# Optimization experiments

Measured on AMD Instinct MI355X. Metric: run time of the kernel, lower is better.

The kernel has to match this reference:

```python
import jax, jax.numpy as jnp
import numpy as np

RES = 32            # input grid resolution
OUT_RES = 64        # after subdivide
C = 128             # channels (== out_channels -> skip is identity)
G = 32              # group-norm groups
N = 8192            # active input voxels
EPS = 1e-5

# 8 child offsets for subdivide, 27 stencil offsets for 3x3x3 submanifold conv
_OFFS8 = np.stack(np.meshgrid([0, 1], [0, 1], [0, 1], indexing='ij'), -1).reshape(-1, 3).astype(np.int32)
_OFFS27 = np.stack(np.meshgrid([-1, 0, 1], [-1, 0, 1], [-1, 0, 1], indexing='ij'), -1).reshape(-1, 3).astype(np.int32)


def group_norm(x, gamma, beta, num_groups=G, eps=EPS):
    # sparse group norm over all active voxels of the (single) sample
    n, c = x.shape
    xg = x.reshape(n, num_groups, c // num_groups)
    mean = xg.mean(axis=(0, 2), keepdims=True)
    var = xg.var(axis=(0, 2), keepdims=True)
    xn = (xg - mean) * jax.lax.rsqrt(var + eps)
    return xn.reshape(n, c) * gamma + beta


def subdivide_coords(coords):
    offs = jnp.asarray(_OFFS8)
    return (coords[:, None, :] * 2 + offs[None, :, :]).reshape(-1, 3)  # [8N, 3]


def subm_conv3d(feats, coords, W, b, grid_res):
    # submanifold 3x3x3 sparse conv: outputs only at active sites
    n = feats.shape[0]
    grid = jnp.full((grid_res, grid_res, grid_res), -1, dtype=jnp.int32)
    grid = grid.at[coords[:, 0], coords[:, 1], coords[:, 2]].set(
        jnp.arange(n, dtype=jnp.int32))
    out = jnp.zeros((n, W.shape[-1]), dtype=feats.dtype)
    for k in range(27):  # fixed small stencil loop
        off = jnp.asarray(_OFFS27[k])
        nb = coords + off
        inb = jnp.all((nb >= 0) & (nb < grid_res), axis=1)
        nbc = jnp.clip(nb, 0, grid_res - 1)
        idx = grid[nbc[:, 0], nbc[:, 1], nbc[:, 2]]
        mask = inb & (idx >= 0)
        g = jnp.where(mask[:, None], feats[jnp.where(mask, idx, 0)], 0.0)
        out = out + g @ W[k]
    return out + b


def setup_inputs() -> dict:
    key = jax.random.key(0)
    ks = jax.random.split(key, 8)
    rng = np.random.default_rng(0)
    flat = rng.choice(RES ** 3, size=N, replace=False)
    coords = np.stack([flat // (RES * RES), (flat // RES) % RES, flat % RES],
                      axis=-1).astype(np.int32)
    feats = jax.random.normal(ks[0], (N, C), dtype=jnp.float32)
    gamma1 = 1.0 + 0.1 * jax.random.normal(ks[1], (C,), dtype=jnp.float32)
    beta1 = 0.1 * jax.random.normal(ks[2], (C,), dtype=jnp.float32)
    W1 = jax.random.normal(ks[3], (27, C, C), dtype=jnp.float32) * 0.05
    b1 = jax.random.normal(ks[4], (C,), dtype=jnp.float32) * 0.05
    gamma2 = 1.0 + 0.1 * jax.random.normal(ks[5], (C,), dtype=jnp.float32)
    beta2 = 0.1 * jax.random.normal(ks[6], (C,), dtype=jnp.float32)
    W2 = jax.random.normal(ks[7], (27, C, C), dtype=jnp.float32) * 0.05
    b2 = jax.random.normal(jax.random.fold_in(key, 99), (C,), dtype=jnp.float32) * 0.05
    return {"feats": feats, "gamma1": gamma1, "beta1": beta1, "W1": W1,
            "b1": b1, "gamma2": gamma2, "beta2": beta2, "W2": W2, "b2": b2,
            "coords": jnp.asarray(coords)}


def reference(feats, gamma1, beta1, W1, b1, gamma2, beta2, W2, b2, coords):
    # act_layers: GroupNorm + SiLU at input resolution
    h = jax.nn.silu(group_norm(feats, gamma1, beta1))
    # subdivide both branch and residual (8 children per voxel)
    new_coords = subdivide_coords(coords)          # [8N, 3] in OUT_RES grid
    h = jnp.repeat(h, 8, axis=0)
    x_sub = jnp.repeat(feats, 8, axis=0)
    # out_layers: conv3 -> GN -> SiLU -> conv3 (submanifold, same active set)
    h = subm_conv3d(h, new_coords, W1, b1, OUT_RES)
    h = jax.nn.silu(group_norm(h, gamma2, beta2))
    h = subm_conv3d(h, new_coords, W2, b2, OUT_RES)
    # skip_connection is Identity since out_channels == channels
    return h + x_sub
```

## Files before the change

kernel.cpp:

```cpp
#include <hip/hip_runtime.h>

#define NPAR   8192
#define NCH    65536
#define RES    32
#define EPS    1e-5f

typedef __attribute__((ext_vector_type(8))) short short8;
typedef __attribute__((ext_vector_type(4))) float floatx4;

__device__ __forceinline__ unsigned short f2bf(float f) {
    union { float f; unsigned u; } v; v.f = f;
    unsigned r = v.u + 0x7fffu + ((v.u >> 16) & 1u);
    return (unsigned short)(r >> 16);
}
__device__ __forceinline__ float bf2f(unsigned short b) {
    union { unsigned u; float f; } v; v.u = ((unsigned)b) << 16;
    return v.f;
}
__device__ __forceinline__ void glds16(const void* g, void* l) {
    __builtin_amdgcn_global_load_lds(
        (__attribute__((address_space(1))) const void*)g,
        (__attribute__((address_space(3))) void*)l, 16, 0, 0);
}
__device__ __forceinline__ int k27_of(int o, int s) {
    return (((o >> 2) & 1) + ((s >> 2) & 1)) * 9 +
           (((o >> 1) & 1) + ((s >> 1) & 1)) * 3 +
           ((o & 1) + (s & 1));
}
__device__ __forceinline__ void axis_dlist(int o, int s, int* d, int& n) {
    if (o == 0) { if (s == 0) { d[0] = -1; n = 1; } else { d[0] = 0; d[1] = 1; n = 2; } }
    else        { if (s == 0) { d[0] = -1; d[1] = 0; n = 2; } else { d[0] = 1; n = 1; } }
}

__global__ void k1_kernel(const int* __restrict__ coords, int* __restrict__ grid32,
                          const float* __restrict__ x, float* __restrict__ sum,
                          float* __restrict__ sq) {
    int b = blockIdx.x;
    int t = threadIdx.x;
    if (b < 32) {
        int p = b * 256 + t;
        grid32[(coords[p*3] << 10) + (coords[p*3+1] << 5) + coords[p*3+2]] = p;
    } else {
        __shared__ float s_sum[32], s_sq[32];
        if (t < 32) { s_sum[t] = 0.0f; s_sq[t] = 0.0f; }
        __syncthreads();
        const float4* x4 = (const float4*)x;
        int total = NPAR * 32;
        int idx0 = (b - 32) * 256 + t;
        int g = idx0 & 31;
        float ls = 0.0f, lq = 0.0f;
        for (int idx = idx0; idx < total; idx += 256 * 256) {
            float4 v = x4[idx];
            ls += v.x + v.y + v.z + v.w;
            lq += v.x * v.x + v.y * v.y + v.z * v.z + v.w * v.w;
        }
        atomicAdd(&s_sum[g], ls);
        atomicAdd(&s_sq[g], lq);
        __syncthreads();
        if (t < 32) { atomicAdd(&sum[t], s_sum[t]); atomicAdd(&sq[t], s_sq[t]); }
    }
}

__global__ void k2_kernel(const int* __restrict__ coords, const int* __restrict__ grid32,
                          int* __restrict__ idx_tab, int* __restrict__ pidx27,
                          const float* __restrict__ W1, const float* __restrict__ W2,
                          unsigned short* __restrict__ Wc1f, unsigned short* __restrict__ Wp2,
                          const float* __restrict__ x, const float* __restrict__ sum,
                          const float* __restrict__ sq, const float* __restrict__ gamma,
                          const float* __restrict__ beta, unsigned short* __restrict__ y) {
    int b = blockIdx.x;
    if (b < 256) {
        int R = b * 256 + threadIdx.x;
        int p = R >> 3, o = R & 7;
        int bx = 2 * coords[p*3]   + ((o >> 2) & 1);
        int by = 2 * coords[p*3+1] + ((o >> 1) & 1);
        int bz = 2 * coords[p*3+2] + (o & 1);
#pragma unroll 1
        for (int k = 0; k < 27; ++k) {
            int fx = bx + k / 9 - 1, fy = by + (k / 3) % 3 - 1, fz = bz + k % 3 - 1;
            int src = -1;
            if ((unsigned)fx < 64u && (unsigned)fy < 64u && (unsigned)fz < 64u) {
                int r = grid32[((fx >> 1) << 10) + ((fy >> 1) << 5) + (fz >> 1)];
                if ((unsigned)r < (unsigned)NPAR)
                    src = (((fx & 1) << 2) + ((fy & 1) << 1) + (fz & 1)) * NPAR + r;
            }
            idx_tab[k * NCH + R] = src;
        }
    } else if (b < 472) {
        int rem = (b - 256) * 256 + threadIdx.x;
        int lane = rem & 63;
        int ks   = (rem >> 6) & 3;
        int nb   = (rem >> 8) & 7;
        int tap  = rem >> 11;
        int n  = nb * 16 + (lane & 15);
        int k0 = ks * 32 + (lane >> 4) * 8;
        unsigned short v[8];
#pragma unroll
        for (int j = 0; j < 8; ++j) v[j] = f2bf(W2[tap * 16384 + (k0 + j) * 128 + n]);
        uint4 pk;
        pk.x = (unsigned)v[0] | ((unsigned)v[1] << 16);
        pk.y = (unsigned)v[2] | ((unsigned)v[3] << 16);
        pk.z = (unsigned)v[4] | ((unsigned)v[5] << 16);
        pk.w = (unsigned)v[6] | ((unsigned)v[7] << 16);
        *(uint4*)&Wp2[(long)rem * 8] = pk;
    } else if (b < 984) {
        int rem = (b - 472) * 256 + threadIdx.x;
        int lane  = rem & 63;
        int ks    = (rem >> 6) & 3;
        int nb    = (rem >> 8) & 7;
        int combo = rem >> 11;
        int o = combo >> 3, s = combo & 7;
        int n  = nb * 16 + (lane & 15);
        int k0 = ks * 32 + (lane >> 4) * 8;
        int d0[2], d1[2], d2[2], n0, n1, n2;
        axis_dlist((o >> 2) & 1, (s >> 2) & 1, d0, n0);
        axis_dlist((o >> 1) & 1, (s >> 1) & 1, d1, n1);
        axis_dlist(o & 1,        s & 1,        d2, n2);
        unsigned short v[8];
#pragma unroll
        for (int j = 0; j < 8; ++j) {
            float acc = 0.0f;
            for (int a = 0; a < n0; ++a)
                for (int bb = 0; bb < n1; ++bb)
                    for (int cc = 0; cc < n2; ++cc) {
                        int kk = (d0[a] + 1) * 9 + (d1[bb] + 1) * 3 + (d2[cc] + 1);
                        acc += W1[kk * 16384 + (k0 + j) * 128 + n];
                    }
            v[j] = f2bf(acc);
        }
        uint4 pk;
        pk.x = (unsigned)v[0] | ((unsigned)v[1] << 16);
        pk.y = (unsigned)v[2] | ((unsigned)v[3] << 16);
        pk.z = (unsigned)v[4] | ((unsigned)v[5] << 16);
        pk.w = (unsigned)v[6] | ((unsigned)v[7] << 16);
        *(uint4*)&Wc1f[(long)rem * 8] = pk;
    } else if (b < 1848) {
        int gid = (b - 984) * 256 + threadIdx.x;
        int k = gid >> 13, p = gid & 8191;
        int nx = coords[p*3]   + k / 9 - 1;
        int ny = coords[p*3+1] + (k / 3) % 3 - 1;
        int nz = coords[p*3+2] + k % 3 - 1;
        int src = -1;
        if ((unsigned)nx < 32u && (unsigned)ny < 32u && (unsigned)nz < 32u) {
            int r = grid32[(nx << 10) + (ny << 5) + nz];
            if ((unsigned)r < (unsigned)NPAR) src = r;
        }
        pidx27[k * NPAR + p] = src;
    } else {
        const float4* x4 = (const float4*)x;
        uint2* y2 = (uint2*)y;
        const float4* g4 = (const float4*)gamma;
        const float4* b4 = (const float4*)beta;
        float cnt = (float)NPAR * 4.0f;
        int total = NPAR * 32;
        for (int idx = (b - 1848) * 256 + threadIdx.x; idx < total; idx += 256 * 256) {
            int c4 = idx & 31;
            float mean = sum[c4] / cnt;
            float var = sq[c4] / cnt - mean * mean;
            float rstd = rsqrtf(var + EPS);
            float4 v = x4[idx];
            float4 gm = g4[c4];
            float4 bt = b4[c4];
            float a[4] = {v.x, v.y, v.z, v.w};
            float gg[4] = {gm.x, gm.y, gm.z, gm.w};
            float bb[4] = {bt.x, bt.y, bt.z, bt.w};
            unsigned short o[4];
#pragma unroll
            for (int i = 0; i < 4; ++i) {
                float tv = (a[i] - mean) * rstd * gg[i] + bb[i];
                o[i] = f2bf(tv / (1.0f + __expf(-tv)));
            }
            uint2 pk;
            pk.x = (unsigned)o[0] | ((unsigned)o[1] << 16);
            pk.y = (unsigned)o[2] | ((unsigned)o[3] << 16);
            y2[idx] = pk;
        }
    }
}

__global__ void gn_apply_bf16_kernel(unsigned short* __restrict__ x,
                                     const float* __restrict__ sum, const float* __restrict__ sq,
                                     const float* __restrict__ gamma, const float* __restrict__ beta,
                                     int nrows) {
    uint2* x2 = (uint2*)x;
    const float4* g4 = (const float4*)gamma;
    const float4* b4 = (const float4*)beta;
    float cnt = (float)nrows * 4.0f;
    int total = nrows * 32;
    for (int idx = blockIdx.x * blockDim.x + threadIdx.x; idx < total;
         idx += gridDim.x * blockDim.x) {
        int c4 = idx & 31;
        float mean = sum[c4] / cnt;
        float var = sq[c4] / cnt - mean * mean;
        float rstd = rsqrtf(var + EPS);
        uint2 pk = x2[idx];
        float a[4] = {bf2f((unsigned short)(pk.x & 0xffff)), bf2f((unsigned short)(pk.x >> 16)),
                      bf2f((unsigned short)(pk.y & 0xffff)), bf2f((unsigned short)(pk.y >> 16))};
        float4 gm = g4[c4];
        float4 bt = b4[c4];
        float gg[4] = {gm.x, gm.y, gm.z, gm.w};
        float bb[4] = {bt.x, bt.y, bt.z, bt.w};
        unsigned short o[4];
#pragma unroll
        for (int i = 0; i < 4; ++i) {
            float tv = (a[i] - mean) * rstd * gg[i] + bb[i];
            o[i] = f2bf(tv / (1.0f + __expf(-tv)));
        }
        pk.x = (unsigned)o[0] | ((unsigned)o[1] << 16);
        pk.y = (unsigned)o[2] | ((unsigned)o[3] << 16);
        x2[idx] = pk;
    }
}

__device__ __forceinline__ void mfma_phase(
    const unsigned short* __restrict__ Abuf, short8 (&bfr)[4][4],
    floatx4 (&acc)[4][4], int wm, int aswz) {
#pragma unroll
    for (int ks = 0; ks < 4; ++ks) {
        short8 afr[4];
#pragma unroll
        for (int mt = 0; mt < 4; ++mt)
            afr[mt] = *(const short8*)&Abuf[(wm << 13) + (mt << 11) + (ks << 9) + aswz];
#pragma unroll
        for (int mt = 0; mt < 4; ++mt)
#pragma unroll
            for (int nt = 0; nt < 4; ++nt)
                acc[mt][nt] = __builtin_amdgcn_mfma_f32_16x16x32_bf16(
                    afr[mt], bfr[nt][ks], acc[mt][nt], 0, 0, 0);
    }
}
__device__ __forceinline__ void loadB(const unsigned short* __restrict__ Wtap,
                                      short8 (&bfr)[4][4], int wn, int lane) {
#pragma unroll
    for (int nt = 0; nt < 4; ++nt)
#pragma unroll
        for (int ks = 0; ks < 4; ++ks)
            bfr[nt][ks] = *(const short8*)&Wtap[(((wn * 4 + nt) << 2) + ks) * 512 + (lane << 3)];
}
__device__ __forceinline__ void stageA(const unsigned short* __restrict__ Ag,
                                       int iv0, int iv1, const unsigned short* zsrc,
                                       unsigned short* __restrict__ buf,
                                       int base0, int base1, int cchOff) {
    const unsigned short* g0 = (iv0 >= 0) ? Ag + (long)iv0 * 128 : zsrc;
    const unsigned short* g1 = (iv1 >= 0) ? Ag + (long)iv1 * 128 : zsrc;
#pragma unroll
    for (int i = 0; i < 4; ++i) glds16(g0 + i * 32 + cchOff, &buf[base0 + i * 512]);
#pragma unroll
    for (int i = 0; i < 4; ++i) glds16(g1 + i * 32 + cchOff, &buf[base1 + i * 512]);
}

__global__ void __launch_bounds__(256, 2) conv1_fold_kernel(
    const unsigned short* __restrict__ Ag, const unsigned short* __restrict__ Wc1f,
    const float* __restrict__ bias, const int* __restrict__ pidx27,
    unsigned short* __restrict__ outp, const float* __restrict__ zpage,
    float* __restrict__ gsum, float* __restrict__ gsq) {
    __shared__ unsigned short A_lds[2][16384];

    int t = threadIdx.x;
    int o  = blockIdx.x & 7;
    int P0 = (blockIdx.x >> 3) << 7;
    const unsigned short* Wb = Wc1f + ((long)o << 17);
    int wv = t >> 6, lane = t & 63, quad = lane >> 4, l16 = lane & 15;
    int wm = wv & 1, wn = wv >> 1;
    int r16 = lane >> 2, cch = lane & 3;
    int c0 = wv * 2, c1 = wv * 2 + 1;
    int row0 = ((c0 >> 2) << 6) + ((c0 & 3) << 4) + r16;
    int row1 = ((c1 >> 2) << 6) + ((c1 & 3) << 4) + r16;
    int base0 = ((c0 >> 2) << 13) + ((c0 & 3) << 11);
    int base1 = ((c1 >> 2) << 13) + ((c1 & 3) << 11);
    int cchOff = (cch ^ ((r16 >> 1) & 3)) << 3;
    int aswz = (l16 << 5) + ((quad ^ ((l16 >> 1) & 3)) << 3);
    const unsigned short* zsrc = (const unsigned short*)zpage;

    floatx4 acc[4][4];
#pragma unroll
    for (int mt = 0; mt < 4; ++mt)
#pragma unroll
        for (int nt = 0; nt < 4; ++nt)
            acc[mt][nt] = (floatx4){0.f, 0.f, 0.f, 0.f};
    short8 bA[4][4], bB[4][4];

    stageA(Ag, pidx27[k27_of(o, 0) * NPAR + P0 + row0],
               pidx27[k27_of(o, 0) * NPAR + P0 + row1], zsrc, A_lds[0], base0, base1, cchOff);
    loadB(Wb, bA, wn, lane);
    int nv0 = pidx27[k27_of(o, 1) * NPAR + P0 + row0];
    int nv1 = pidx27[k27_of(o, 1) * NPAR + P0 + row1];
    __syncthreads();

#pragma unroll 1
    for (int s = 0; s < 8; s += 2) {
        stageA(Ag, nv0, nv1, zsrc, A_lds[1], base0, base1, cchOff);
        loadB(Wb + ((long)(s + 1) << 14), bB, wn, lane);
        if (s + 2 < 8) {
            nv0 = pidx27[k27_of(o, s + 2) * NPAR + P0 + row0];
            nv1 = pidx27[k27_of(o, s + 2) * NPAR + P0 + row1];
        }
        mfma_phase(A_lds[0], bA, acc, wm, aswz);
        __syncthreads();
        if (s + 2 < 8) {
            stageA(Ag, nv0, nv1, zsrc, A_lds[0], base0, base1, cchOff);
            loadB(Wb + ((long)(s + 2) << 14), bA, wn, lane);
            if (s + 3 < 8) {
                nv0 = pidx27[k27_of(o, s + 3) * NPAR + P0 + row0];
                nv1 = pidx27[k27_of(o, s + 3) * NPAR + P0 + row1];
            }
        }
        mfma_phase(A_lds[1], bB, acc, wm, aswz);
        __syncthreads();
    }

    float s_[4] = {0.f, 0.f, 0.f, 0.f}, q_[4] = {0.f, 0.f, 0.f, 0.f};
#pragma unroll
    for (int nt = 0; nt < 4; ++nt) {
        int col = wn * 64 + nt * 16 + l16;
        float bv = bias[col];
#pragma unroll
        for (int mt = 0; mt < 4; ++mt) {
#pragma unroll
            for (int r = 0; r < 4; ++r) {
                int prow = wm * 64 + mt * 16 + quad * 4 + r;
                long R = (long)o * NPAR + P0 + prow;
                float v = acc[mt][nt][r] + bv;
                unsigned short u = f2bf(v);
                outp[R * 128 + col] = u;
                float vr = bf2f(u);
                s_[nt] += vr;
                q_[nt] += vr * vr;
            }
        }
    }
    float* sred = (float*)A_lds;
    if (t < 64) sred[t] = 0.0f;
    __syncthreads();
#pragma unroll
    for (int nt = 0; nt < 4; ++nt) {
        int g = (wn * 64 + nt * 16 + l16) >> 2;
        atomicAdd(&sred[g], s_[nt]);
        atomicAdd(&sred[32 + g], q_[nt]);
    }
    __syncthreads();
    if (t < 32) { atomicAdd(&gsum[t], sred[t]); atomicAdd(&gsq[t], sred[32 + t]); }
}

__global__ void __launch_bounds__(256, 2) conv2_kernel(
    const unsigned short* __restrict__ Ag, const unsigned short* __restrict__ Wp,
    const float* __restrict__ bias, const int* __restrict__ idx_tab,
    const float* __restrict__ resid, float* __restrict__ outp,
    const float* __restrict__ zpage) {
    __shared__ unsigned short A_lds[2][16384];

    int t = threadIdx.x;
    int R0 = blockIdx.x * 128;
    int wv = t >> 6, lane = t & 63, quad = lane >> 4, l16 = lane & 15;
    int wm = wv & 1, wn = wv >> 1;
    int r16 = lane >> 2, cch = lane & 3;
    int c0 = wv * 2, c1 = wv * 2 + 1;
    int row0 = ((c0 >> 2) << 6) + ((c0 & 3) << 4) + r16;
    int row1 = ((c1 >> 2) << 6) + ((c1 & 3) << 4) + r16;
    int base0 = ((c0 >> 2) << 13) + ((c0 & 3) << 11);
    int base1 = ((c1 >> 2) << 13) + ((c1 & 3) << 11);
    int cchOff = (cch ^ ((r16 >> 1) & 3)) << 3;
    int aswz = (l16 << 5) + ((quad ^ ((l16 >> 1) & 3)) << 3);
    const unsigned short* zsrc = (const unsigned short*)zpage;

    floatx4 acc[4][4];
#pragma unroll
    for (int mt = 0; mt < 4; ++mt)
#pragma unroll
        for (int nt = 0; nt < 4; ++nt)
            acc[mt][nt] = (floatx4){0.f, 0.f, 0.f, 0.f};
    short8 bA[4][4], bB[4][4];

    stageA(Ag, idx_tab[R0 + row0], idx_tab[R0 + row1], zsrc, A_lds[0], base0, base1, cchOff);
    loadB(Wp, bA, wn, lane);
    int nv0 = idx_tab[NCH + R0 + row0], nv1 = idx_tab[NCH + R0 + row1];
    __syncthreads();

#pragma unroll 1
    for (int k = 0; k < 27; k += 2) {
        if (k + 1 < 27) {
            stageA(Ag, nv0, nv1, zsrc, A_lds[1], base0, base1, cchOff);
            loadB(Wp + ((long)(k + 1) << 14), bB, wn, lane);
            if (k + 2 < 27) {
                nv0 = idx_tab[(k + 2) * NCH + R0 + row0];
                nv1 = idx_tab[(k + 2) * NCH + R0 + row1];
            }
        }
        mfma_phase(A_lds[0], bA, acc, wm, aswz);
        __syncthreads();
        if (k + 1 < 27) {
            if (k + 2 < 27) {
                stageA(Ag, nv0, nv1, zsrc, A_lds[0], base0, base1, cchOff);
                loadB(Wp + ((long)(k + 2) << 14), bA, wn, lane);
                if (k + 3 < 27) {
                    nv0 = idx_tab[(k + 3) * NCH + R0 + row0];
                    nv1 = idx_tab[(k + 3) * NCH + R0 + row1];
                }
            }
            mfma_phase(A_lds[1], bB, acc, wm, aswz);
            __syncthreads();
        }
    }

#pragma unroll
    for (int nt = 0; nt < 4; ++nt) {
        int col = wn * 64 + nt * 16 + l16;
        float bv = bias[col];
#pragma unroll
        for (int mt = 0; mt < 4; ++mt) {
#pragma unroll
            for (int r = 0; r < 4; ++r) {
                int row = wm * 64 + mt * 16 + quad * 4 + r;
                long R = (long)R0 + row;
                float v = acc[mt][nt][r] + bv + resid[(R >> 3) * 128 + col];
                outp[R * 128 + col] = v;
            }
        }
    }
}

extern "C" void kernel_launch(void* const* d_in, const int* in_sizes, int n_in,
                              void* d_out, int out_size, void* d_ws, size_t ws_size,
                              hipStream_t stream) {
    const float* feats  = (const float*)d_in[0];
    const float* gamma1 = (const float*)d_in[1];
    const float* beta1  = (const float*)d_in[2];
    const float* W1     = (const float*)d_in[3];
    const float* b1     = (const float*)d_in[4];
    const float* gamma2 = (const float*)d_in[5];
    const float* beta2  = (const float*)d_in[6];
    const float* W2     = (const float*)d_in[7];
    const float* b2     = (const float*)d_in[8];
    const int*   coords = (const int*)d_in[9];
    float* out = (float*)d_out;

    char* ws = (char*)d_ws;
    unsigned short* h0b  = (unsigned short*)(ws);
    unsigned short* h1b  = (unsigned short*)(ws + (2u << 20));
    unsigned short* Wc1f = (unsigned short*)(ws + (18u << 20));
    unsigned short* Wp2  = (unsigned short*)(ws + (20u << 20));
    int*   grid32        = (int*)  (ws + (21u << 20));
    float* stats         = (float*)(ws + (21u << 20) + 131072);
    float* zpage         = (float*)(ws + (21u << 20) + 131072 + 512);
    int*   idx_tab       = (int*)  (ws + (22u << 20));
    int*   pidx27        = (int*)  (ws + (30u << 20));

    hipMemsetAsync(stats, 0, 1024, stream);

    k1_kernel<<<288, 256, 0, stream>>>(coords, grid32, feats, stats + 0, stats + 32);
    k2_kernel<<<2104, 256, 0, stream>>>(coords, grid32, idx_tab, pidx27,
                                        W1, W2, Wc1f, Wp2,
                                        feats, stats + 0, stats + 32, gamma1, beta1, h0b);

    conv1_fold_kernel<<<8 * (NPAR / 128), 256, 0, stream>>>(h0b, Wc1f, b1, pidx27,
                                                            h1b, zpage,
                                                            stats + 64, stats + 96);

    gn_apply_bf16_kernel<<<1024, 256, 0, stream>>>(h1b, stats + 64, stats + 96, gamma2, beta2, NCH);

    conv2_kernel<<<NCH / 128, 256, 0, stream>>>(h1b, Wp2, b2, idx_tab,
                                                feats, out, zpage);
}
```

Baseline: 206.9 us.

## Derive fine neighbor table from parent stencil and relax conv barriers with partial vmcnt

The index-building kernel now computes each parent's 27 coarse neighbors once and derives all 8 children's 27 fine-grid neighbor indices from them. This replaces separate per-child grid lookups and the separate pidx27 block range, so the launch shrinks. In both conv kernels, __syncthreads is replaced by an s_waitcnt vmcnt(16) plus s_barrier, with sched barriers, so the just-issued prefetch loads can stay in flight across the phase barrier. The partial vmcnt is correct only if the count of outstanding loads matches what the pipeline issues. A wrong count would cause data races on the LDS buffers.

```diff
diff --git a/kernel.cpp b/kernel.cpp
--- a/kernel.cpp
+++ b/kernel.cpp
@@ -30,6 +30,11 @@
 __device__ __forceinline__ void axis_dlist(int o, int s, int* d, int& n) {
     if (o == 0) { if (s == 0) { d[0] = -1; n = 1; } else { d[0] = 0; d[1] = 1; n = 2; } }
     else        { if (s == 0) { d[0] = -1; d[1] = 0; n = 2; } else { d[0] = 1; n = 1; } }
+}
+
+__device__ __forceinline__ void phase_sync() {
+    asm volatile("s_waitcnt vmcnt(16)\n\ts_barrier" ::: "memory");
+    __builtin_amdgcn_sched_barrier(0);
 }
 
 __global__ void k1_kernel(const int* __restrict__ coords, int* __restrict__ grid32,
@@ -69,25 +74,41 @@
                           const float* __restrict__ sq, const float* __restrict__ gamma,
                           const float* __restrict__ beta, unsigned short* __restrict__ y) {
     int b = blockIdx.x;
-    if (b < 256) {
-        int R = b * 256 + threadIdx.x;
-        int p = R >> 3, o = R & 7;
-        int bx = 2 * coords[p*3]   + ((o >> 2) & 1);
-        int by = 2 * coords[p*3+1] + ((o >> 1) & 1);
-        int bz = 2 * coords[p*3+2] + (o & 1);
-#pragma unroll 1
+    if (b < 32) {
+        int p = b * 256 + threadIdx.x;
+        int cx = coords[p*3], cy = coords[p*3+1], cz = coords[p*3+2];
+        int r27[27];
+#pragma unroll
         for (int k = 0; k < 27; ++k) {
-            int fx = bx + k / 9 - 1, fy = by + (k / 3) % 3 - 1, fz = bz + k % 3 - 1;
-            int src = -1;
-            if ((unsigned)fx < 64u && (unsigned)fy < 64u && (unsigned)fz < 64u) {
-                int r = grid32[((fx >> 1) << 10) + ((fy >> 1) << 5) + (fz >> 1)];
-                if ((unsigned)r < (unsigned)NPAR)
-                    src = (((fx & 1) << 2) + ((fy & 1) << 1) + (fz & 1)) * NPAR + r;
-            }
-            idx_tab[k * NCH + R] = src;
-        }
-    } else if (b < 472) {
-        int rem = (b - 256) * 256 + threadIdx.x;
+            int nx = cx + k / 9 - 1, ny = cy + (k / 3) % 3 - 1, nz = cz + k % 3 - 1;
+            int r = -1;
+            if ((unsigned)nx < 32u && (unsigned)ny < 32u && (unsigned)nz < 32u) {
+                int g = grid32[(nx << 10) + (ny << 5) + nz];
+                if ((unsigned)g < (unsigned)NPAR) r = g;
+            }
+            r27[k] = r;
+            pidx27[k * NPAR + p] = r;
+        }
+#pragma unroll
+        for (int k = 0; k < 27; ++k) {
+            const int dx = k / 9 - 1, dy = (k / 3) % 3 - 1, dz = k % 3 - 1;
+            int v[8];
+#pragma unroll
+            for (int o = 0; o < 8; ++o) {
+                const int ex = ((o >> 2) & 1) + dx;
+                const int ey = ((o >> 1) & 1) + dy;
+                const int ez = (o & 1) + dz;
+                const int ptap = ((ex >> 1) + 1) * 9 + ((ey >> 1) + 1) * 3 + ((ez >> 1) + 1);
+                const int slot = ((ex & 1) << 2) + ((ey & 1) << 1) + (ez & 1);
+                int r = r27[ptap];
+                v[o] = (r >= 0) ? slot * NPAR + r : -1;
+            }
+            int4* dst = (int4*)&idx_tab[k * NCH + p * 8];
+            dst[0] = make_int4(v[0], v[1], v[2], v[3]);
+            dst[1] = make_int4(v[4], v[5], v[6], v[7]);
+        }
+    } else if (b < 248) {
+        int rem = (b - 32) * 256 + threadIdx.x;
         int lane = rem & 63;
         int ks   = (rem >> 6) & 3;
         int nb   = (rem >> 8) & 7;
@@ -103,8 +124,8 @@
         pk.z = (unsigned)v[4] | ((unsigned)v[5] << 16);
         pk.w = (unsigned)v[6] | ((unsigned)v[7] << 16);
         *(uint4*)&Wp2[(long)rem * 8] = pk;
-    } else if (b < 984) {
-        int rem = (b - 472) * 256 + threadIdx.x;
+    } else if (b < 760) {
+        int rem = (b - 248) * 256 + threadIdx.x;
         int lane  = rem & 63;
         int ks    = (rem >> 6) & 3;
         int nb    = (rem >> 8) & 7;
@@ -134,18 +155,6 @@
         pk.z = (unsigned)v[4] | ((unsigned)v[5] << 16);
         pk.w = (unsigned)v[6] | ((unsigned)v[7] << 16);
         *(uint4*)&Wc1f[(long)rem * 8] = pk;
-    } else if (b < 1848) {
-        int gid = (b - 984) * 256 + threadIdx.x;
-        int k = gid >> 13, p = gid & 8191;
-        int nx = coords[p*3]   + k / 9 - 1;
-        int ny = coords[p*3+1] + (k / 3) % 3 - 1;
-        int nz = coords[p*3+2] + k % 3 - 1;
-        int src = -1;
-        if ((unsigned)nx < 32u && (unsigned)ny < 32u && (unsigned)nz < 32u) {
-            int r = grid32[(nx << 10) + (ny << 5) + nz];
-            if ((unsigned)r < (unsigned)NPAR) src = r;
-        }
-        pidx27[k * NPAR + p] = src;
     } else {
         const float4* x4 = (const float4*)x;
         uint2* y2 = (uint2*)y;
@@ -153,7 +162,7 @@
         const float4* b4 = (const float4*)beta;
         float cnt = (float)NPAR * 4.0f;
         int total = NPAR * 32;
-        for (int idx = (b - 1848) * 256 + threadIdx.x; idx < total; idx += 256 * 256) {
+        for (int idx = (b - 760) * 256 + threadIdx.x; idx < total; idx += 256 * 256) {
             int c4 = idx & 31;
             float mean = sum[c4] / cnt;
             float var = sq[c4] / cnt - mean * mean;
@@ -247,6 +256,7 @@
     for (int i = 0; i < 4; ++i) glds16(g0 + i * 32 + cchOff, &buf[base0 + i * 512]);
 #pragma unroll
     for (int i = 0; i < 4; ++i) glds16(g1 + i * 32 + cchOff, &buf[base1 + i * 512]);
+    __builtin_amdgcn_sched_barrier(0);
 }
 
 __global__ void __launch_bounds__(256, 2) conv1_fold_kernel(
@@ -285,7 +295,7 @@
     loadB(Wb, bA, wn, lane);
     int nv0 = pidx27[k27_of(o, 1) * NPAR + P0 + row0];
     int nv1 = pidx27[k27_of(o, 1) * NPAR + P0 + row1];
-    __syncthreads();
+    phase_sync();
 
 #pragma unroll 1
     for (int s = 0; s < 8; s += 2) {
@@ -296,7 +306,7 @@
             nv1 = pidx27[k27_of(o, s + 2) * NPAR + P0 + row1];
         }
         mfma_phase(A_lds[0], bA, acc, wm, aswz);
-        __syncthreads();
+        phase_sync();
         if (s + 2 < 8) {
             stageA(Ag, nv0, nv1, zsrc, A_lds[0], base0, base1, cchOff);
             loadB(Wb + ((long)(s + 2) << 14), bA, wn, lane);
@@ -306,7 +316,7 @@
             }
         }
         mfma_phase(A_lds[1], bB, acc, wm, aswz);
-        __syncthreads();
+        phase_sync();
     }
 
     float s_[4] = {0.f, 0.f, 0.f, 0.f}, q_[4] = {0.f, 0.f, 0.f, 0.f};
@@ -374,7 +384,7 @@
     stageA(Ag, idx_tab[R0 + row0], idx_tab[R0 + row1], zsrc, A_lds[0], base0, base1, cchOff);
     loadB(Wp, bA, wn, lane);
     int nv0 = idx_tab[NCH + R0 + row0], nv1 = idx_tab[NCH + R0 + row1];
-    __syncthreads();
+    phase_sync();
 
 #pragma unroll 1
     for (int k = 0; k < 27; k += 2) {
@@ -387,7 +397,7 @@
             }
         }
         mfma_phase(A_lds[0], bA, acc, wm, aswz);
-        __syncthreads();
+        phase_sync();
         if (k + 1 < 27) {
             if (k + 2 < 27) {
                 stageA(Ag, nv0, nv1, zsrc, A_lds[0], base0, base1, cchOff);
@@ -398,7 +408,7 @@
                 }
             }
             mfma_phase(A_lds[1], bB, acc, wm, aswz);
-            __syncthreads();
+            phase_sync();
         }
     }
 
@@ -448,7 +458,7 @@
     hipMemsetAsync(stats, 0, 1024, stream);
 
     k1_kernel<<<288, 256, 0, stream>>>(coords, grid32, feats, stats + 0, stats + 32);
-    k2_kernel<<<2104, 256, 0, stream>>>(coords, grid32, idx_tab, pidx27,
+    k2_kernel<<<1016, 256, 0, stream>>>(coords, grid32, idx_tab, pidx27,
                                         W1, W2, Wc1f, Wp2,
                                         feats, stats + 0, stats + 32, gamma1, beta1, h0b);
 
```

After: 213.9 us. 3.4% more time.
